# Performance work log

Hardware: AMD Instinct MI355X
Metric: run time of the kernel (lower is better)

## Reference

```python
import jax, jax.numpy as jnp
import numpy as np

N_HEADS = 8
N_GROUPS = 32
EPS = 1e-6


def setup_inputs() -> dict:
    key = jax.random.key(0)
    ks = jax.random.split(key, 8)
    b, c, n, K = 2, 512, 1024, 64
    x = jax.random.normal(ks[0], (b, c, n), dtype=jnp.float32)
    valid_mask = jax.random.randint(ks[1], (n, K), 0, 2, dtype=jnp.int32)
    # ensure every query attends to at least one key (avoids all--inf softmax rows)
    valid_mask = valid_mask.at[:, 0].set(1)
    attend_idx = jax.random.randint(ks[2], (n, K), 0, n, dtype=jnp.int64)
    scale = 0.03
    return {
        "x": x,
        "valid_mask": valid_mask,
        "attend_idx": attend_idx,
        "gn_gamma": jnp.ones((c,), jnp.float32),
        "gn_beta": jnp.zeros((c,), jnp.float32),
        "wq": jax.random.normal(ks[3], (c, c), jnp.float32) * scale,
        "bq": jnp.zeros((c,), jnp.float32),
        "wk": jax.random.normal(ks[4], (c, c), jnp.float32) * scale,
        "bk": jnp.zeros((c,), jnp.float32),
        "wv": jax.random.normal(ks[5], (c, c), jnp.float32) * scale,
        "bv": jnp.zeros((c,), jnp.float32),
        "wo": jax.random.normal(ks[6], (c, c), jnp.float32) * scale,
        "bo": jnp.zeros((c,), jnp.float32),
    }


def _group_norm(x, gamma, beta):
    b, c, n = x.shape
    xr = x.reshape(b, N_GROUPS, c // N_GROUPS, n)
    mu = xr.mean(axis=(2, 3), keepdims=True)
    var = xr.var(axis=(2, 3), keepdims=True)
    h = ((xr - mu) * jax.lax.rsqrt(var + EPS)).reshape(b, c, n)
    return h * gamma[None, :, None] + beta[None, :, None]


def reference(x, valid_mask, attend_idx, gn_gamma, gn_beta,
              wq, bq, wk, bk, wv, bv, wo, bo):
    b, c, n = x.shape
    H = N_HEADS
    dh = c // H
    h = _group_norm(x, gn_gamma, gn_beta)
    # 1x1 Conv1d == per-node linear projection
    proj = lambda w, bias: jnp.einsum('oc,bcn->bon', w, h) + bias[None, :, None]
    q = proj(wq, bq).reshape(b, H, dh, n)
    k = proj(wk, bk).reshape(b, H, dh, n)
    v = proj(wv, bv).reshape(b, H, dh, n)
    # gather attendable keys/values per query: [b, H, nq, K, dh]
    kT = jnp.transpose(k, (0, 1, 3, 2))  # [b, H, n, dh]
    vT = jnp.transpose(v, (0, 1, 3, 2))
    keys = jnp.take(kT, attend_idx, axis=2)
    vals = jnp.take(vT, attend_idx, axis=2)
    # NOTE: sparse_forward uses beta=1 (no 1/sqrt(dh) scaling)
    w = jnp.einsum('bhqkc,bhcq->bhqk', keys, q)
    w = jnp.where(valid_mask[None, None] == 0, -jnp.inf, w)
    w = jax.nn.softmax(w, axis=-1)
    o = jnp.einsum('bhqk,bhqkc->bhqc', w, vals)  # [b, H, n, dh]
    # permute(0,3,1,2).reshape(b,c,n): channel layout is (dh, H)
    o = jnp.transpose(o, (0, 3, 1, 2)).reshape(b, c, n)
    out = x + jnp.einsum('oc,bcn->bon', wo, o) + bo[None, :, None]
    return out
```

## Files before the change

### kernel.cpp

```cpp
#include <hip/hip_runtime.h>
#include <hip/hip_bf16.h>

#define B_   2
#define C_   512
#define N_   1024
#define KK_  64
#define H_   8
#define DH_  64
#define NG_  32
#define MQKV 1536

typedef __attribute__((ext_vector_type(8))) short short8;
typedef __attribute__((ext_vector_type(4))) float f32x4;

__device__ __forceinline__ float ldf(const void* p, size_t i, int isbf) {
  return isbf ? __bfloat162float(((const __hip_bfloat16*)p)[i])
              : ((const float*)p)[i];
}
__device__ __forceinline__ unsigned short f2bfu(float f) {
  __hip_bfloat16 h = __float2bfloat16(f);
  unsigned short u; __builtin_memcpy(&u, &h, 2); return u;
}
__device__ __forceinline__ float bfu2f(unsigned short u) {
  return __uint_as_float(((unsigned)u) << 16);
}
__device__ __forceinline__ int detect_bf(const void* gamma) {
  return ((const unsigned*)gamma)[0] == 0x3F803F80u;
}
__device__ __forceinline__ uint4 ld8_bf(const void* w, size_t off, int isbf) {
  if (isbf) return *(const uint4*)((const unsigned short*)w + off);
  float4 a = *(const float4*)((const float*)w + off);
  float4 b = *(const float4*)((const float*)w + off + 4);
  uint4 u;
  u.x = (unsigned)f2bfu(a.x) | ((unsigned)f2bfu(a.y) << 16);
  u.y = (unsigned)f2bfu(a.z) | ((unsigned)f2bfu(a.w) << 16);
  u.z = (unsigned)f2bfu(b.x) | ((unsigned)f2bfu(b.y) << 16);
  u.w = (unsigned)f2bfu(b.z) | ((unsigned)f2bfu(b.w) << 16);
  return u;
}
__device__ __forceinline__ void dma16(const void* g, void* l) {
  __builtin_amdgcn_global_load_lds(
      (const __attribute__((address_space(1))) unsigned*)g,
      (__attribute__((address_space(3))) unsigned*)l, 16, 0, 0);
}

__global__ __launch_bounds__(256) void conv_k(
    const void* x, const void* wq, const void* wk, const void* wv, const void* wo,
    const void* gamma, unsigned short* __restrict__ wqkvS,
    unsigned short* __restrict__ woS, float2* __restrict__ part) {
  const int isbf = detect_bf(gamma);
  const int tid = threadIdx.x;
  const int idx = blockIdx.x * 256 + tid;
  {
    int m = idx >> 9, c = idx & 511;
    const void* src = (m < 512) ? wq : (m < 1024 ? wk : wv);
    wqkvS[idx] = f2bfu(ldf(src, (size_t)(m & 511) * C_ + c, isbf));
  }
  if (woS != nullptr && blockIdx.x >= 1024 && blockIdx.x < 2048) {
    int i2 = (blockIdx.x - 1024) * 256 + tid;
    woS[i2] = f2bfu(ldf(wo, i2, isbf));
  }

  __shared__ float ssum[256], ssq[256];
  if (blockIdx.x < 256) {
    const size_t base = (size_t)blockIdx.x * 4096;
    float sum = 0.f, sq = 0.f;
    if (isbf) {
      const uint4* p = (const uint4*)((const unsigned short*)x + base);
      for (int t = tid; t < 512; t += 256) {
        uint4 u = p[t];
        unsigned wv4[4] = {u.x, u.y, u.z, u.w};
#pragma unroll
        for (int q = 0; q < 4; q++) {
          float a = __uint_as_float(wv4[q] << 16);
          float b = __uint_as_float(wv4[q] & 0xffff0000u);
          sum += a + b; sq += a * a + b * b;
        }
      }
    } else {
      const float4* p = (const float4*)((const float*)x + base);
      for (int t = tid; t < 1024; t += 256) {
        float4 v = p[t];
        sum += v.x + v.y + v.z + v.w;
        sq  += v.x * v.x + v.y * v.y + v.z * v.z + v.w * v.w;
      }
    }
    ssum[tid] = sum; ssq[tid] = sq;
    __syncthreads();
    for (int s = 128; s > 0; s >>= 1) {
      if (tid < s) { ssum[tid] += ssum[tid + s]; ssq[tid] += ssq[tid + s]; }
      __syncthreads();
    }
    if (tid == 0) part[blockIdx.x] = make_float2(ssum[0], ssq[0]);
  }
}

__global__ __launch_bounds__(256) void gn_apply_k(
    const void* x, const void* gamma, const void* beta,
    const float2* __restrict__ part, unsigned short* __restrict__ hT) {
  const int isbf = detect_bf(gamma);
  const int n0 = blockIdx.x * 64, c0 = blockIdx.y * 64, b = blockIdx.z;
  const int tid = threadIdx.x;
  __shared__ unsigned short Lt[64][72];
#pragma unroll
  for (int p = 0; p < 2; p++) {
    int idx = tid + p * 256;
    int cl = idx >> 3, seg = idx & 7;
    int c = c0 + cl;
    int bgi = (b * NG_ + (c >> 4)) * 4;
    float2 p0 = part[bgi], p1 = part[bgi + 1], p2 = part[bgi + 2], p3 = part[bgi + 3];
    float S = p0.x + p1.x + p2.x + p3.x;
    float Q = p0.y + p1.y + p2.y + p3.y;
    float mu = S * (1.f / 16384.f);
    float rs = rsqrtf(fmaxf(Q * (1.f / 16384.f) - mu * mu, 0.f) + 1e-6f);
    float ga = ldf(gamma, c, isbf), be = ldf(beta, c, isbf);
    size_t srow = ((size_t)b * C_ + c) * N_ + n0 + seg * 8;
    float v[8];
    if (isbf) {
      uint4 u = *(const uint4*)((const unsigned short*)x + srow);
      v[0] = __uint_as_float(u.x << 16); v[1] = __uint_as_float(u.x & 0xffff0000u);
      v[2] = __uint_as_float(u.y << 16); v[3] = __uint_as_float(u.y & 0xffff0000u);
      v[4] = __uint_as_float(u.z << 16); v[5] = __uint_as_float(u.z & 0xffff0000u);
      v[6] = __uint_as_float(u.w << 16); v[7] = __uint_as_float(u.w & 0xffff0000u);
    } else {
      float4 a = *(const float4*)((const float*)x + srow);
      float4 bb = *(const float4*)((const float*)x + srow + 4);
      v[0] = a.x; v[1] = a.y; v[2] = a.z; v[3] = a.w;
      v[4] = bb.x; v[5] = bb.y; v[6] = bb.z; v[7] = bb.w;
    }
#pragma unroll
    for (int e = 0; e < 8; e++)
      Lt[seg * 8 + e][cl] = f2bfu((v[e] - mu) * rs * ga + be);
  }
  __syncthreads();
#pragma unroll
  for (int p = 0; p < 2; p++) {
    int idx = tid + p * 256;
    int nl = idx >> 3, seg = idx & 7;
    uint4 v = *(const uint4*)&Lt[nl][seg * 8];
    *(uint4*)&hT[((size_t)b * N_ + n0 + nl) * C_ + c0 + seg * 8] = v;
  }
}

__global__ __launch_bounds__(256) void qkv_gemm_k(
    const unsigned short* __restrict__ wqkvS, const unsigned short* __restrict__ hT,
    const void* bq, const void* bk, const void* bv, const void* gamma,
    unsigned short* __restrict__ qkv) {
  const int isbf = detect_bf(gamma);
  __shared__ short As[8192], Bs[8192];
  const int tid = threadIdx.x;
  const int lane = tid & 63, wave = tid >> 6;
  const int wm = wave >> 1, wn = wave & 1;
  const int n0 = blockIdx.x * 64;
  const int m0 = blockIdx.y * 64;
  const int b  = blockIdx.z;
  const unsigned short* Bbase = hT + (size_t)b * N_ * C_;
  const void* bsrc = (m0 < 512) ? bq : (m0 < 1024 ? bk : bv);

  const int r = lane & 15, kh = (lane >> 4) << 3;
  const size_t arow = (size_t)(m0 + wave * 16 + r) * C_;
  const size_t brow = (size_t)(n0 + wave * 16 + r) * C_;
  short* Ad = &As[wave * 512];
  short* Bd = &Bs[wave * 512];

  f32x4 acc[2][2];
#pragma unroll
  for (int i = 0; i < 2; i++)
#pragma unroll
    for (int j = 0; j < 2; j++) acc[i][j] = (f32x4){0.f, 0.f, 0.f, 0.f};

#define STAGE_Q(bufv, k0v)                                              \
  { dma16(&wqkvS[arow + (k0v) + kh],      Ad + (bufv) * 4096);          \
    dma16(&wqkvS[arow + (k0v) + 32 + kh], Ad + (bufv) * 4096 + 2048);   \
    dma16(&Bbase[brow + (k0v) + kh],      Bd + (bufv) * 4096);          \
    dma16(&Bbase[brow + (k0v) + 32 + kh], Bd + (bufv) * 4096 + 2048); }

  STAGE_Q(0, 0);
  __syncthreads();
  int buf = 0;
  for (int t = 0; t < 8; ++t) {
    if (t < 7) STAGE_Q(buf ^ 1, (t + 1) * 64);
#pragma unroll
    for (int s = 0; s < 2; ++s) {
      const short8* Av = (const short8*)&As[buf * 4096 + s * 2048];
      const short8* Bv = (const short8*)&Bs[buf * 4096 + s * 2048];
      short8 af[2], bg[2];
#pragma unroll
      for (int i = 0; i < 2; i++) af[i] = Av[(wm * 2 + i) * 64 + lane];
#pragma unroll
      for (int j = 0; j < 2; j++) bg[j] = Bv[(wn * 2 + j) * 64 + lane];
#pragma unroll
      for (int i = 0; i < 2; i++)
#pragma unroll
        for (int j = 0; j < 2; j++)
          acc[i][j] = __builtin_amdgcn_mfma_f32_16x16x32_bf16(af[i], bg[j], acc[i][j], 0, 0, 0);
    }
    __syncthreads();
    buf ^= 1;
  }
#undef STAGE_Q

  const int mb = m0 + wm * 32;
#pragma unroll
  for (int i = 0; i < 2; i++) {
    int mrow0 = mb + i * 16 + ((lane >> 4) << 2);
    int mat = mrow0 >> 9, head = (mrow0 >> 6) & 7, d0 = mrow0 & 63;
    int br = mrow0 & 511;
    float b0 = ldf(bsrc, br, isbf),     b1 = ldf(bsrc, br + 1, isbf);
    float b2 = ldf(bsrc, br + 2, isbf), b3 = ldf(bsrc, br + 3, isbf);
#pragma unroll
    for (int j = 0; j < 2; j++) {
      int n = n0 + wn * 32 + j * 16 + (lane & 15);
      uint2 st;
      st.x = (unsigned)f2bfu(acc[i][j][0] + b0) | ((unsigned)f2bfu(acc[i][j][1] + b1) << 16);
      st.y = (unsigned)f2bfu(acc[i][j][2] + b2) | ((unsigned)f2bfu(acc[i][j][3] + b3) << 16);
      size_t dst = (size_t)mat * ((size_t)B_ * H_ * N_ * DH_) +
                   (((size_t)b * H_ + head) * N_ + n) * DH_ + d0;
      *(uint2*)&qkv[dst] = st;
    }
  }
}

__global__ __launch_bounds__(512) void attn_k(
    const unsigned short* __restrict__ qkv, const void* aidx,
    const int* __restrict__ vmask, unsigned short* __restrict__ ocT) {
  const int tid = threadIdx.x, w = tid >> 6, lane = tid & 63;
  const int b = blockIdx.x >> 10, qi = blockIdx.x & 1023;

  const unsigned* aw = (const unsigned*)aidx;
  unsigned long long bal = __ballot(aw[2 * lane + 1] != 0u);
  const int is64 = (bal == 0ull);

  __shared__ float qs[8][64];
  __shared__ float wl[8][64];
  __shared__ int   il[8][64];
  __shared__ unsigned short olds[512];

  const size_t S = (size_t)B_ * H_ * N_ * DH_;
  const unsigned short* qT = qkv;
  const unsigned short* kT = qkv + S;
  const unsigned short* vT = qkv + 2 * S;
  const size_t bh = ((size_t)b * H_ + w) * N_;

  qs[w][lane] = bfu2f(qT[(bh + qi) * DH_ + lane]);
  const size_t ai = (size_t)qi * KK_ + lane;
  int idx = is64 ? (int)((const long long*)aidx)[ai] : ((const int*)aidx)[ai];
  idx &= (N_ - 1);
  const int valid = vmask[ai];
  __threadfence_block();

  const uint4* k4 = (const uint4*)&kT[(bh + idx) * DH_];
  float s = 0.f;
#pragma unroll
  for (int j2 = 0; j2 < 8; j2++) {
    uint4 u = k4[j2];
    const float* q8 = &qs[w][j2 * 8];
    s += __uint_as_float(u.x << 16) * q8[0] + __uint_as_float(u.x & 0xffff0000u) * q8[1]
       + __uint_as_float(u.y << 16) * q8[2] + __uint_as_float(u.y & 0xffff0000u) * q8[3]
       + __uint_as_float(u.z << 16) * q8[4] + __uint_as_float(u.z & 0xffff0000u) * q8[5]
       + __uint_as_float(u.w << 16) * q8[6] + __uint_as_float(u.w & 0xffff0000u) * q8[7];
  }
  s = valid ? s : -INFINITY;

  float m = s;
#pragma unroll
  for (int off = 32; off > 0; off >>= 1) m = fmaxf(m, __shfl_xor(m, off));
  float e = valid ? __expf(s - m) : 0.f;
  float sum = e;
#pragma unroll
  for (int off = 32; off > 0; off >>= 1) sum += __shfl_xor(sum, off);

  wl[w][lane] = (sum > 0.f) ? (e / sum) : 0.f;
  il[w][lane] = idx;
  __threadfence_block();

  const unsigned short* vbase = vT + bh * DH_;
  const int half = lane >> 5, dhp = lane & 31;
  float a0 = 0.f, a1 = 0.f;
#pragma unroll 8
  for (int ki = 0; ki < KK_ / 2; ki++) {
    int key = 2 * ki + half;
    float wgt = wl[w][key];
    unsigned uv = *(const unsigned*)&vbase[(size_t)il[w][key] * DH_ + 2 * dhp];
    a0 += wgt * __uint_as_float(uv << 16);
    a1 += wgt * __uint_as_float(uv & 0xffff0000u);
  }
  a0 += __shfl_xor(a0, 32);
  a1 += __shfl_xor(a1, 32);
  if (half == 0) {
    olds[(2 * dhp) * H_ + w]     = f2bfu(a0);
    olds[(2 * dhp + 1) * H_ + w] = f2bfu(a1);
  }
  __syncthreads();
  if (tid < 64) {
    uint4 vv = *(const uint4*)&olds[tid * 8];
    *(uint4*)&ocT[((size_t)b * N_ + qi) * C_ + tid * 8] = vv;
  }
}

__global__ __launch_bounds__(256) void out_gemm_k(
    const void* wo, const unsigned short* __restrict__ woS,
    const unsigned short* __restrict__ ocT,
    const void* bo, const void* __restrict__ x,
    const void* gamma, void* __restrict__ out) {
  const int isbf = detect_bf(gamma);
  __shared__ short As[8192], Bs[8192];
  const int tid = threadIdx.x;
  const int lane = tid & 63, wave = tid >> 6;
  const int wm = wave >> 1, wn = wave & 1;
  const int n0 = blockIdx.x * 64;
  const int m0 = blockIdx.y * 64;
  const int b  = blockIdx.z;
  const unsigned short* Bbase = ocT + (size_t)b * N_ * C_;
  const unsigned short* asrc = woS ? woS : (isbf ? (const unsigned short*)wo : nullptr);

  const int r = lane & 15, kh = (lane >> 4) << 3;
  const size_t arow = (size_t)(m0 + wave * 16 + r) * C_;
  const size_t brow = (size_t)(n0 + wave * 16 + r) * C_;
  short* Ad = &As[wave * 512];
  short* Bd = &Bs[wave * 512];

  f32x4 acc[2][2];
#pragma unroll
  for (int i = 0; i < 2; i++)
#pragma unroll
    for (int j = 0; j < 2; j++) acc[i][j] = (f32x4){0.f, 0.f, 0.f, 0.f};

#define STAGE_O(bufv, k0v)                                                        \
  { if (asrc) {                                                                   \
      dma16(&asrc[arow + (k0v) + kh],      Ad + (bufv) * 4096);                   \
      dma16(&asrc[arow + (k0v) + 32 + kh], Ad + (bufv) * 4096 + 2048);            \
    } else {                                                                      \
      *(uint4*)&As[(bufv) * 4096 + tid * 8]        = ld8_bf(wo, arow + (k0v) + kh, 0);      \
      *(uint4*)&As[(bufv) * 4096 + 2048 + tid * 8] = ld8_bf(wo, arow + (k0v) + 32 + kh, 0); \
    }                                                                             \
    dma16(&Bbase[brow + (k0v) + kh],      Bd + (bufv) * 4096);                    \
    dma16(&Bbase[brow + (k0v) + 32 + kh], Bd + (bufv) * 4096 + 2048); }

  STAGE_O(0, 0);
  __syncthreads();
  int buf = 0;
  for (int t = 0; t < 8; ++t) {
    if (t < 7) STAGE_O(buf ^ 1, (t + 1) * 64);
#pragma unroll
    for (int s = 0; s < 2; ++s) {
      const short8* Av = (const short8*)&As[buf * 4096 + s * 2048];
      const short8* Bv = (const short8*)&Bs[buf * 4096 + s * 2048];
      short8 af[2], bg[2];
#pragma unroll
      for (int i = 0; i < 2; i++) af[i] = Av[(wm * 2 + i) * 64 + lane];
#pragma unroll
      for (int j = 0; j < 2; j++) bg[j] = Bv[(wn * 2 + j) * 64 + lane];
#pragma unroll
      for (int i = 0; i < 2; i++)
#pragma unroll
        for (int j = 0; j < 2; j++)
          acc[i][j] = __builtin_amdgcn_mfma_f32_16x16x32_bf16(bg[j], af[i], acc[i][j], 0, 0, 0);
    }
    __syncthreads();
    buf ^= 1;
  }
#undef STAGE_O

#pragma unroll
  for (int i = 0; i < 2; i++) {
    int m = m0 + wm * 32 + i * 16 + (lane & 15);
    float bias = ldf(bo, m, isbf);
#pragma unroll
    for (int j = 0; j < 2; j++) {
      int nb = n0 + wn * 32 + j * 16 + ((lane >> 4) << 2);
      size_t oi = ((size_t)b * C_ + m) * N_ + nb;
      if (isbf) {
        const unsigned short* xp = (const unsigned short*)x;
        uint2 xv = *(const uint2*)&xp[oi];
        uint2 st;
        st.x = (unsigned)f2bfu(bfu2f((unsigned short)(xv.x & 0xffff)) + acc[i][j][0] + bias) |
               ((unsigned)f2bfu(bfu2f((unsigned short)(xv.x >> 16)) + acc[i][j][1] + bias) << 16);
        st.y = (unsigned)f2bfu(bfu2f((unsigned short)(xv.y & 0xffff)) + acc[i][j][2] + bias) |
               ((unsigned)f2bfu(bfu2f((unsigned short)(xv.y >> 16)) + acc[i][j][3] + bias) << 16);
        *(uint2*)&((unsigned short*)out)[oi] = st;
      } else {
        const float* xp = (const float*)x;
        float4 xv = *(const float4*)&xp[oi];
        float4 st;
        st.x = xv.x + acc[i][j][0] + bias;
        st.y = xv.y + acc[i][j][1] + bias;
        st.z = xv.z + acc[i][j][2] + bias;
        st.w = xv.w + acc[i][j][3] + bias;
        *(float4*)&((float*)out)[oi] = st;
      }
    }
  }
}

extern "C" void kernel_launch(void* const* d_in, const int* in_sizes, int n_in,
                              void* d_out, int out_size, void* d_ws, size_t ws_size,
                              hipStream_t stream) {
  const void* x     = d_in[0];
  const int*  vmask = (const int*)d_in[1];
  const void* aidx  = d_in[2];
  const void* gamma = d_in[3];
  const void* beta  = d_in[4];
  const void* wq = d_in[5],  *bq = d_in[6];
  const void* wk = d_in[7],  *bk = d_in[8];
  const void* wv = d_in[9],  *bv = d_in[10];
  const void* wo = d_in[11], *bo = d_in[12];

  unsigned short* qkv = (unsigned short*)d_ws;
  unsigned short* hT  = qkv + (size_t)3 * B_ * H_ * N_ * DH_;
  unsigned short* ocT = hT;
  unsigned short* wqkvS = (unsigned short*)d_out;
  float2* part = (float2*)((char*)d_out + (size_t)MQKV * C_ * 2);
  unsigned short* woS = nullptr;
  if (ws_size >= ((size_t)8 << 20) + (size_t)C_ * C_ * 2)
    woS = (unsigned short*)((char*)d_ws + ((size_t)8 << 20));

  conv_k<<<(MQKV * C_) / 256, 256, 0, stream>>>(x, wq, wk, wv, wo, gamma,
                                                wqkvS, woS, part);
  gn_apply_k<<<dim3(N_ / 64, C_ / 64, B_), 256, 0, stream>>>(x, gamma, beta, part, hT);
  qkv_gemm_k<<<dim3(N_ / 64, MQKV / 64, B_), 256, 0, stream>>>(
      wqkvS, hT, bq, bk, bv, gamma, qkv);
  attn_k<<<B_ * N_, 512, 0, stream>>>(qkv, aidx, vmask, ocT);
  out_gemm_k<<<dim3(N_ / 64, C_ / 64, B_), 256, 0, stream>>>(
      wo, woS, ocT, bo, x, gamma, d_out);
}
```

Measured before the change: 139.9 us.

## Vectorize weight conversion and coalesce key gathers in sparse attention

The weight-conversion kernel now has each thread convert 8 elements with 16-byte loads and stores, so the launch shrinks from 3072 blocks to 512. The attention kernel now splits each key row across 8 lanes, each reading a 16-byte chunk, and reduces the partial dot products with shuffles. This replaces one lane reading a whole 128-byte row on its own, so key gathers become more coalesced. The cost is extra shuffle reductions and a gather of indices and validity through LDS.

```diff
diff --git a/kernel.cpp b/kernel.cpp
--- a/kernel.cpp
+++ b/kernel.cpp
@@ -43,6 +43,14 @@
       (const __attribute__((address_space(1))) unsigned*)g,
       (__attribute__((address_space(3))) unsigned*)l, 16, 0, 0);
 }
+__device__ __forceinline__ float dot8(uint4 kv, const float* qf) {
+  float s;
+  s  = __uint_as_float(kv.x << 16) * qf[0] + __uint_as_float(kv.x & 0xffff0000u) * qf[1];
+  s += __uint_as_float(kv.y << 16) * qf[2] + __uint_as_float(kv.y & 0xffff0000u) * qf[3];
+  s += __uint_as_float(kv.z << 16) * qf[4] + __uint_as_float(kv.z & 0xffff0000u) * qf[5];
+  s += __uint_as_float(kv.w << 16) * qf[6] + __uint_as_float(kv.w & 0xffff0000u) * qf[7];
+  return s;
+}
 
 __global__ __launch_bounds__(256) void conv_k(
     const void* x, const void* wq, const void* wk, const void* wv, const void* wo,
@@ -50,15 +58,15 @@
     unsigned short* __restrict__ woS, float2* __restrict__ part) {
   const int isbf = detect_bf(gamma);
   const int tid = threadIdx.x;
-  const int idx = blockIdx.x * 256 + tid;
-  {
-    int m = idx >> 9, c = idx & 511;
+  const int t8 = blockIdx.x * 256 + tid;
+  if (t8 < (MQKV * C_) / 8) {
+    int e0 = t8 * 8;
+    int m = e0 >> 9, c0 = e0 & 511;
     const void* src = (m < 512) ? wq : (m < 1024 ? wk : wv);
-    wqkvS[idx] = f2bfu(ldf(src, (size_t)(m & 511) * C_ + c, isbf));
-  }
-  if (woS != nullptr && blockIdx.x >= 1024 && blockIdx.x < 2048) {
-    int i2 = (blockIdx.x - 1024) * 256 + tid;
-    woS[i2] = f2bfu(ldf(wo, i2, isbf));
+    *(uint4*)&wqkvS[e0] = ld8_bf(src, (size_t)(m & 511) * C_ + c0, isbf);
+  } else if (woS != nullptr && t8 < (MQKV * C_) / 8 + (C_ * C_) / 8) {
+    int e0 = (t8 - (MQKV * C_) / 8) * 8;
+    *(uint4*)&woS[e0] = ld8_bf(wo, e0, isbf);
   }
 
   __shared__ float ssum[256], ssq[256];
@@ -226,14 +234,15 @@
     const int* __restrict__ vmask, unsigned short* __restrict__ ocT) {
   const int tid = threadIdx.x, w = tid >> 6, lane = tid & 63;
   const int b = blockIdx.x >> 10, qi = blockIdx.x & 1023;
+  const int kg = lane >> 3, dq = lane & 7;
 
   const unsigned* aw = (const unsigned*)aidx;
   unsigned long long bal = __ballot(aw[2 * lane + 1] != 0u);
   const int is64 = (bal == 0ull);
 
-  __shared__ float qs[8][64];
   __shared__ float wl[8][64];
   __shared__ int   il[8][64];
+  __shared__ int   vl[8][64];
   __shared__ unsigned short olds[512];
 
   const size_t S = (size_t)B_ * H_ * N_ * DH_;
@@ -242,36 +251,43 @@
   const unsigned short* vT = qkv + 2 * S;
   const size_t bh = ((size_t)b * H_ + w) * N_;
 
-  qs[w][lane] = bfu2f(qT[(bh + qi) * DH_ + lane]);
+  uint4 qv = *(const uint4*)&qT[(bh + qi) * DH_ + dq * 8];
+  float qf[8];
+  qf[0] = __uint_as_float(qv.x << 16); qf[1] = __uint_as_float(qv.x & 0xffff0000u);
+  qf[2] = __uint_as_float(qv.y << 16); qf[3] = __uint_as_float(qv.y & 0xffff0000u);
+  qf[4] = __uint_as_float(qv.z << 16); qf[5] = __uint_as_float(qv.z & 0xffff0000u);
+  qf[6] = __uint_as_float(qv.w << 16); qf[7] = __uint_as_float(qv.w & 0xffff0000u);
+
   const size_t ai = (size_t)qi * KK_ + lane;
   int idx = is64 ? (int)((const long long*)aidx)[ai] : ((const int*)aidx)[ai];
   idx &= (N_ - 1);
-  const int valid = vmask[ai];
+  il[w][lane] = idx;
+  vl[w][lane] = vmask[ai];
   __threadfence_block();
 
-  const uint4* k4 = (const uint4*)&kT[(bh + idx) * DH_];
-  float s = 0.f;
-#pragma unroll
-  for (int j2 = 0; j2 < 8; j2++) {
-    uint4 u = k4[j2];
-    const float* q8 = &qs[w][j2 * 8];
-    s += __uint_as_float(u.x << 16) * q8[0] + __uint_as_float(u.x & 0xffff0000u) * q8[1]
-       + __uint_as_float(u.y << 16) * q8[2] + __uint_as_float(u.y & 0xffff0000u) * q8[3]
-       + __uint_as_float(u.z << 16) * q8[4] + __uint_as_float(u.z & 0xffff0000u) * q8[5]
-       + __uint_as_float(u.w << 16) * q8[6] + __uint_as_float(u.w & 0xffff0000u) * q8[7];
-  }
-  s = valid ? s : -INFINITY;
-
-  float m = s;
+  float own = 0.f;
+#pragma unroll
+  for (int p = 0; p < 8; p++) {
+    int key = p * 8 + kg;
+    int ix = il[w][key];
+    uint4 kv = *(const uint4*)&kT[(bh + ix) * DH_ + dq * 8];
+    float s = dot8(kv, qf);
+    s += __shfl_xor(s, 1); s += __shfl_xor(s, 2); s += __shfl_xor(s, 4);
+    if (dq == p) own = s;
+  }
+  const int keyown = dq * 8 + kg;
+  const int valid = vl[w][keyown];
+  float sc = valid ? own : -INFINITY;
+
+  float m = sc;
 #pragma unroll
   for (int off = 32; off > 0; off >>= 1) m = fmaxf(m, __shfl_xor(m, off));
-  float e = valid ? __expf(s - m) : 0.f;
+  float e = valid ? __expf(sc - m) : 0.f;
   float sum = e;
 #pragma unroll
   for (int off = 32; off > 0; off >>= 1) sum += __shfl_xor(sum, off);
 
-  wl[w][lane] = (sum > 0.f) ? (e / sum) : 0.f;
-  il[w][lane] = idx;
+  wl[w][keyown] = (sum > 0.f) ? (e / sum) : 0.f;
   __threadfence_block();
 
   const unsigned short* vbase = vT + bh * DH_;
@@ -415,8 +431,7 @@
   if (ws_size >= ((size_t)8 << 20) + (size_t)C_ * C_ * 2)
     woS = (unsigned short*)((char*)d_ws + ((size_t)8 << 20));
 
-  conv_k<<<(MQKV * C_) / 256, 256, 0, stream>>>(x, wq, wk, wv, wo, gamma,
-                                                wqkvS, woS, part);
+  conv_k<<<512, 256, 0, stream>>>(x, wq, wk, wv, wo, gamma, wqkvS, woS, part);
   gn_apply_k<<<dim3(N_ / 64, C_ / 64, B_), 256, 0, stream>>>(x, gamma, beta, part, hT);
   qkv_gemm_k<<<dim3(N_ / 64, MQKV / 64, B_), 256, 0, stream>>>(
       wqkvS, hT, bq, bk, bv, gamma, qkv);
```

After: 130.8 us. 6.5% less time.
